# Kernel tuning notes

Measured on AMD Instinct MI355X. Metric: run time of the kernel, lower is better.

Reference implementation:

```python
import jax, jax.numpy as jnp
import numpy as np

NEG_SLOPE = 0.01  # torch LeakyReLU default

def setup_inputs() -> dict:
    key = jax.random.key(0)
    ks = jax.random.split(key, 16)
    B, T = 256, 168
    LAG, LAT, WS, H = 168, 128, 64, 1024
    def lin(kw, kb, out_f, in_f):
        bound = 1.0 / np.sqrt(in_f)
        W = jax.random.uniform(kw, (out_f, in_f), jnp.float32, -bound, bound)
        b = jax.random.uniform(kb, (out_f,), jnp.float32, -bound, bound)
        return W, b
    W1, b1 = lin(ks[0], ks[1], 64, LAG)
    W2, b2 = lin(ks[2], ks[3], LAT, 64)
    W3, b3 = lin(ks[4], ks[5], H, LAT)
    bound = 1.0 / np.sqrt(H)
    Wih = jax.random.uniform(ks[6], (3 * H, WS), jnp.float32, -bound, bound)
    Whh = jax.random.uniform(ks[7], (3 * H, H), jnp.float32, -bound, bound)
    bih = jax.random.uniform(ks[8], (3 * H,), jnp.float32, -bound, bound)
    bhh = jax.random.uniform(ks[9], (3 * H,), jnp.float32, -bound, bound)
    Wo, bo = lin(ks[10], ks[11], 1, H)
    lag = jax.random.normal(ks[12], (B, LAG), jnp.float32)
    curr = jax.random.normal(ks[13], (T, B, WS), jnp.float32)
    return dict(lag=lag, curr=curr, W1=W1, b1=b1, W2=W2, b2=b2, W3=W3, b3=b3,
                Wih=Wih, Whh=Whh, bih=bih, bhh=bhh, Wo=Wo, bo=bo)

def _leaky(x):
    return jnp.where(x >= 0, x, NEG_SLOPE * x)

def reference(lag, curr, W1, b1, W2, b2, W3, b3, Wih, Whh, bih, bhh, Wo, bo):
    # Encoder MLP: lag -> 64 -> latent -> hidden (leaky relu after first two)
    h = _leaky(lag @ W1.T + b1)
    h = _leaky(h @ W2.T + b2)
    h0 = h @ W3.T + b3  # [B, H]
    H = h0.shape[-1]

    def step(h_t, x_t):
        gi = x_t @ Wih.T + bih          # [B, 3H]
        gh = h_t @ Whh.T + bhh          # [B, 3H]
        ir, iz, inn = jnp.split(gi, 3, axis=-1)
        hr, hz, hn = jnp.split(gh, 3, axis=-1)
        r = jax.nn.sigmoid(ir + hr)
        z = jax.nn.sigmoid(iz + hz)
        n = jnp.tanh(inn + r * hn)
        h_new = (1.0 - z) * n + z * h_t
        return h_new, h_new

    _, hs = jax.lax.scan(step, h0, curr)          # hs: [T, B, H]
    preds = jnp.squeeze(hs @ Wo.T + bo, -1)       # [T, B]
    return preds.T                                 # [B, T]
```

## Files before the change

kernel.cpp:

```cpp
#include <hip/hip_runtime.h>
#include <hip/hip_bf16.h>
#include <cstdint>
#include <cstddef>

typedef _Float16 half8 __attribute__((ext_vector_type(8)));
typedef _Float16 half4 __attribute__((ext_vector_type(4)));
typedef float floatx4 __attribute__((ext_vector_type(4)));
typedef unsigned long long u64;

#define B_ 256
#define T_ 168
#define H_ 1024
#define WS_ 64
#define LAG_ 168
#define LAT_ 128

__device__ __forceinline__ float fast_sigmoid(float x) {
    return __builtin_amdgcn_rcpf(1.f + __expf(-x));
}
__device__ __forceinline__ float fast_tanh(float x) {
    return 1.f - 2.f * __builtin_amdgcn_rcpf(__expf(2.f * x) + 1.f);
}

__global__ void cvt_all(const float4* __restrict__ a, half4* __restrict__ da, int na,
                        const float4* __restrict__ b, half4* __restrict__ db, int nb,
                        const float4* __restrict__ c, half4* __restrict__ dc, int nc) {
    int i = blockIdx.x * blockDim.x + threadIdx.x;
    const float4* s;
    half4* d;
    int j = i;
    if (j < na) { s = a; d = da; }
    else {
        j -= na;
        if (j < nb) { s = b; d = db; }
        else {
            j -= nb;
            if (j >= nc) return;
            s = c; d = dc;
        }
    }
    float4 v = s[j];
    half4 o;
    o[0] = (_Float16)v.x; o[1] = (_Float16)v.y;
    o[2] = (_Float16)v.z; o[3] = (_Float16)v.w;
    d[j] = o;
}

__global__ void enc_fused(const float* __restrict__ lag,
                          const float* __restrict__ W1, const float* __restrict__ b1,
                          const float* __restrict__ W2, const float* __restrict__ b2,
                          const float* __restrict__ W3, const float* __restrict__ b3,
                          float* __restrict__ hprev32, _Float16* __restrict__ h0f16) {
    __shared__ float lrow[LAG_];
    __shared__ float l1[64];
    __shared__ float l2[LAT_];
    const int r = blockIdx.x, tid = threadIdx.x;
    if (tid < LAG_) lrow[tid] = lag[(size_t)r * LAG_ + tid];
    __syncthreads();
    if (tid < 64) {
        const float* w = W1 + (size_t)tid * LAG_;
        float s = b1[tid];
        for (int k = 0; k < LAG_; ++k) s += lrow[k] * w[k];
        l1[tid] = (s >= 0.f) ? s : 0.01f * s;
    }
    __syncthreads();
    if (tid < LAT_) {
        const float* w = W2 + (size_t)tid * 64;
        float s = b2[tid];
        for (int k = 0; k < 64; ++k) s += l1[k] * w[k];
        l2[tid] = (s >= 0.f) ? s : 0.01f * s;
    }
    __syncthreads();
    for (int j = tid; j < H_; j += 256) {
        const float* w = W3 + (size_t)j * LAT_;
        float acc = b3[j];
        #pragma unroll 8
        for (int k = 0; k < LAT_; ++k) acc += l2[k] * w[k];
        hprev32[(size_t)r * H_ + j] = acc;
        h0f16[(size_t)r * H_ + j]   = (_Float16)acc;
    }
}

__global__ __launch_bounds__(256, 1) void gru_persistent(
    _Float16* __restrict__ hbuf,
    const float* __restrict__ hprev32, const _Float16* __restrict__ whh16,
    const _Float16* __restrict__ wih16, const _Float16* __restrict__ x16,
    const float* __restrict__ bih, const float* __restrict__ bhh,
    const float* __restrict__ Wo, float* __restrict__ partials,
    unsigned* __restrict__ bar)
{
    __shared__ __align__(16) _Float16 Ash[16 * 1032];
    __shared__ __align__(16) _Float16 Wsh[192 * 72];
    __shared__ __align__(16) _Float16 Hsh[4 * 256];

    const int tid  = threadIdx.x;
    const int w    = tid >> 6;
    const int lane = tid & 63;
    const int m16  = lane & 15;
    const int quad = lane >> 4;
    const int pi   = blockIdx.x & 15;
    const int qi   = blockIdx.x >> 4;
    const int pi16 = pi << 4;
    const int u    = (qi << 6) + (w << 4) + m16;

    for (int idx = tid; idx < 1536; idx += 256) {
        int rowl = idx >> 3, ch = idx & 7;
        int g = rowl >> 6, ru = rowl & 63;
        *(uint4*)(&Wsh[rowl * 72 + (ch << 3)]) =
            *(const uint4*)(wih16 + (size_t)(((g << 10) + (qi << 6) + ru) << 6) + (ch << 3));
    }

    half8 br[32], bz[32], bn[32];
    {
        const _Float16* p0 = whh16 + ((size_t)u << 10) + (quad << 3);
        const _Float16* p1 = whh16 + ((size_t)(H_ + u) << 10) + (quad << 3);
        const _Float16* p2 = whh16 + ((size_t)(2 * H_ + u) << 10) + (quad << 3);
        #pragma unroll
        for (int c = 0; c < 32; ++c) br[c] = *(const half8*)(p0 + (c << 5));
        #pragma unroll
        for (int c = 0; c < 32; ++c) bz[c] = *(const half8*)(p1 + (c << 5));
        #pragma unroll
        for (int c = 0; c < 32; ++c) bn[c] = *(const half8*)(p2 + (c << 5));
    }

    const float b_r  = bih[u]          + bhh[u];
    const float b_z  = bih[H_ + u]     + bhh[H_ + u];
    const float b_in = bih[2 * H_ + u];
    const float b_hn = bhh[2 * H_ + u];
    const float wo_u = Wo[u];

    float hreg[4];
    #pragma unroll
    for (int i = 0; i < 4; ++i)
        hreg[i] = hprev32[((size_t)(pi16 + (quad << 2) + i) << 10) + u];

    __syncthreads();

    unsigned* flag_self       = bar + (((pi << 4) | qi) << 4);
    const unsigned* flag_peer = bar + (((pi << 4) | (lane & 15)) << 4);
    const int srow = tid >> 4;
    const int sch  = tid & 15;
    const int prow = lane >> 2;
    const int pc4  = lane & 3;

    for (int t = 0; t < T_; ++t) {
        const _Float16* hsrc = hbuf + (size_t)(t & 3) * (B_ * H_);
        _Float16*       hdst = hbuf + (size_t)((t + 1) & 3) * (B_ * H_);

        half8 ax0 = *(const half8*)(x16 + (((size_t)t << 8) + pi16 + m16) * WS_ + (quad << 3));
        half8 ax1 = *(const half8*)(x16 + (((size_t)t << 8) + pi16 + m16) * WS_ + 32 + (quad << 3));

        const unsigned need = (unsigned)t;
        u64 rdy = 0;

        while ((rdy & 0xFFFFull) != 0xFFFFull) {
            unsigned f = 0;
            if (lane < 16)
                f = __hip_atomic_load(flag_peer, __ATOMIC_RELAXED, __HIP_MEMORY_SCOPE_AGENT);
            rdy |= __ballot(f >= need);
            if ((rdy & 0xFFFFull) != 0xFFFFull) __builtin_amdgcn_s_sleep(1);
        }

        u64 va[4][4];
        {
            const _Float16* s = hsrc + ((size_t)(pi16 + srow) << 10) + (sch << 4);
            #pragma unroll
            for (int g = 0; g < 4; ++g) {
                #pragma unroll
                for (int k = 0; k < 4; ++k)
                    va[g][k] = __hip_atomic_load((const u64*)(s + (g << 8) + (k << 2)),
                                                 __ATOMIC_RELAXED, __HIP_MEMORY_SCOPE_AGENT);
            }
        }

        floatx4 acc_r  = {b_r,  b_r,  b_r,  b_r };
        floatx4 acc_z  = {b_z,  b_z,  b_z,  b_z };
        floatx4 acc_in = {b_in, b_in, b_in, b_in};
        floatx4 acc_hn = {b_hn, b_hn, b_hn, b_hn};

        {
            half8 p0 = *(const half8*)(&Wsh[((w << 4) + m16) * 72        + (quad << 3)]);
            half8 p1 = *(const half8*)(&Wsh[(64 + (w << 4) + m16) * 72   + (quad << 3)]);
            half8 p2 = *(const half8*)(&Wsh[(128 + (w << 4) + m16) * 72  + (quad << 3)]);
            acc_r  = __builtin_amdgcn_mfma_f32_16x16x32_f16(ax0, p0, acc_r,  0, 0, 0);
            acc_z  = __builtin_amdgcn_mfma_f32_16x16x32_f16(ax0, p1, acc_z,  0, 0, 0);
            acc_in = __builtin_amdgcn_mfma_f32_16x16x32_f16(ax0, p2, acc_in, 0, 0, 0);
            half8 q0 = *(const half8*)(&Wsh[((w << 4) + m16) * 72        + 32 + (quad << 3)]);
            half8 q1 = *(const half8*)(&Wsh[(64 + (w << 4) + m16) * 72   + 32 + (quad << 3)]);
            half8 q2 = *(const half8*)(&Wsh[(128 + (w << 4) + m16) * 72  + 32 + (quad << 3)]);
            acc_r  = __builtin_amdgcn_mfma_f32_16x16x32_f16(ax1, q0, acc_r,  0, 0, 0);
            acc_z  = __builtin_amdgcn_mfma_f32_16x16x32_f16(ax1, q1, acc_z,  0, 0, 0);
            acc_in = __builtin_amdgcn_mfma_f32_16x16x32_f16(ax1, q2, acc_in, 0, 0, 0);
        }

        {
            _Float16* dbase = &Ash[srow * 1032 + (sch << 4)];
            #pragma unroll
            for (int g = 0; g < 4; ++g) {
                _Float16* d = dbase + (g << 8);
                *(u64*)(d + 0)  = va[g][0];
                *(u64*)(d + 4)  = va[g][1];
                *(u64*)(d + 8)  = va[g][2];
                *(u64*)(d + 12) = va[g][3];
            }
        }
        __syncthreads();

        #pragma unroll
        for (int c = 0; c < 32; ++c) {
            half8 a = *(const half8*)(&Ash[m16 * 1032 + (c << 5) + (quad << 3)]);
            acc_r  = __builtin_amdgcn_mfma_f32_16x16x32_f16(a, br[c], acc_r,  0, 0, 0);
            acc_z  = __builtin_amdgcn_mfma_f32_16x16x32_f16(a, bz[c], acc_z,  0, 0, 0);
            acc_hn = __builtin_amdgcn_mfma_f32_16x16x32_f16(a, bn[c], acc_hn, 0, 0, 0);
        }

        float pv[4];
        #pragma unroll
        for (int i = 0; i < 4; ++i) {
            float rg = fast_sigmoid(acc_r[i]);
            float zg = fast_sigmoid(acc_z[i]);
            float ng = fast_tanh(acc_in[i] + rg * acc_hn[i]);
            float hn2 = (1.f - zg) * ng + zg * hreg[i];
            hreg[i] = hn2;
            pv[i] = hn2 * wo_u;
            Hsh[(w << 8) + ((quad << 2) + i) * 16 + m16] = (_Float16)hn2;
        }
        __threadfence_block();
        {
            u64 hv = *(const u64*)(&Hsh[(w << 8) + prow * 16 + (pc4 << 2)]);
            __hip_atomic_store(
                (u64*)(hdst + ((size_t)(pi16 + prow) << 10) + (qi << 6) + (w << 4) + (pc4 << 2)),
                hv, __ATOMIC_RELAXED, __HIP_MEMORY_SCOPE_AGENT);
        }
        #pragma unroll
        for (int m = 1; m < 16; m <<= 1) {
            #pragma unroll
            for (int i = 0; i < 4; ++i) pv[i] += __shfl_xor(pv[i], m);
        }
        asm volatile("s_waitcnt vmcnt(0)" ::: "memory");
        __syncthreads();
        if (tid == 0)
            __hip_atomic_store(flag_self, (unsigned)(t + 1),
                               __ATOMIC_RELAXED, __HIP_MEMORY_SCOPE_AGENT);
        if (m16 == 0) {
            #pragma unroll
            for (int i = 0; i < 4; ++i)
                partials[((size_t)(t << 6) + (qi << 2) + w) * 256 + pi16 + (quad << 2) + i] = pv[i];
        }
    }
}

__global__ void out_reduce(const float* __restrict__ partials, const float* __restrict__ bo,
                           float* __restrict__ out) {
    int t = blockIdx.x, r = threadIdx.x;
    float s = 0.f;
    #pragma unroll
    for (int k = 0; k < 64; ++k) s += partials[((size_t)(t << 6) + k) * 256 + r];
    out[(size_t)r * T_ + t] = s + bo[0];
}

extern "C" void kernel_launch(void* const* d_in, const int* in_sizes, int n_in,
                              void* d_out, int out_size, void* d_ws, size_t ws_size,
                              hipStream_t stream) {
    const float* lag  = (const float*)d_in[0];
    const float* curr = (const float*)d_in[1];
    const float* W1   = (const float*)d_in[2];
    const float* b1   = (const float*)d_in[3];
    const float* W2   = (const float*)d_in[4];
    const float* b2   = (const float*)d_in[5];
    const float* W3   = (const float*)d_in[6];
    const float* b3   = (const float*)d_in[7];
    const float* Wih  = (const float*)d_in[8];
    const float* Whh  = (const float*)d_in[9];
    const float* bih  = (const float*)d_in[10];
    const float* bhh  = (const float*)d_in[11];
    const float* Wo   = (const float*)d_in[12];
    const float* bo   = (const float*)d_in[13];
    float* out = (float*)d_out;

    char* ws = (char*)d_ws;
    size_t off = 0;
    auto alloc = [&](size_t bytes) -> void* {
        void* p = ws + off;
        off += (bytes + 255) & ~(size_t)255;
        return p;
    };
    _Float16* whh16 = (_Float16*)alloc((size_t)3 * H_ * H_ * 2);
    _Float16* wih16 = (_Float16*)alloc((size_t)3 * H_ * WS_ * 2);
    _Float16* x16   = (_Float16*)alloc((size_t)T_ * B_ * WS_ * 2);
    _Float16* hbuf  = (_Float16*)alloc((size_t)4 * B_ * H_ * 2);
    float* hprev32  = (float*)alloc((size_t)B_ * H_ * 4);
    float* partials = (float*)alloc((size_t)T_ * B_ * 64 * 4);
    unsigned* bar   = (unsigned*)alloc(81920);

    hipMemsetAsync(bar, 0, 81920, stream);

    const int na = 3 * H_ * H_ / 4;
    const int nb = 3 * H_ * WS_ / 4;
    const int nc = T_ * B_ * WS_ / 4;
    const int ntot = na + nb + nc;
    cvt_all<<<(ntot + 255) / 256, 256, 0, stream>>>(
        (const float4*)Whh, (half4*)whh16, na,
        (const float4*)Wih, (half4*)wih16, nb,
        (const float4*)curr, (half4*)x16, nc);

    enc_fused<<<B_, 256, 0, stream>>>(lag, W1, b1, W2, b2, W3, b3, hprev32, hbuf);

    gru_persistent<<<dim3(256), dim3(256), 0, stream>>>(
        hbuf, hprev32, whh16, wih16, x16, bih, bhh, Wo, partials, bar);

    out_reduce<<<T_, B_, 0, stream>>>(partials, bo, out);
}
```

Measured before the change: 876.7 us.

## Replace per-step flag barrier with sentinel-valued hidden-state ring buffer

Allocates a full T+1 slot ring of hidden states pre-filled with 0xFF sentinels, so consumers poll the data itself instead of waiting on producer flags. This removes the separate flag store/load round trip per step and double-buffers the LDS staging tile. A fallback kernel used when workspace is too small pipelines flag waits per 256-column chunk and streams the n-gate weights from global memory instead of holding them in registers. The cost is a large memset of the ring each call (about 88 MB), and a reliance on no valid fp16 quad equalling the sentinel pattern.

```diff
diff --git a/kernel.cpp b/kernel.cpp
--- a/kernel.cpp
+++ b/kernel.cpp
@@ -14,6 +14,7 @@
 #define WS_ 64
 #define LAG_ 168
 #define LAT_ 128
+#define SENT 0xFFFFFFFFFFFFFFFFull
 
 __device__ __forceinline__ float fast_sigmoid(float x) {
     return __builtin_amdgcn_rcpf(1.f + __expf(-x));
@@ -81,15 +82,14 @@
     }
 }
 
-__global__ __launch_bounds__(256, 1) void gru_persistent(
-    _Float16* __restrict__ hbuf,
+__global__ __launch_bounds__(256, 1) void gru_sentinel(
+    _Float16* __restrict__ hring,
     const float* __restrict__ hprev32, const _Float16* __restrict__ whh16,
     const _Float16* __restrict__ wih16, const _Float16* __restrict__ x16,
     const float* __restrict__ bih, const float* __restrict__ bhh,
-    const float* __restrict__ Wo, float* __restrict__ partials,
-    unsigned* __restrict__ bar)
+    const float* __restrict__ Wo, float* __restrict__ partials)
 {
-    __shared__ __align__(16) _Float16 Ash[16 * 1032];
+    __shared__ __align__(16) _Float16 Ash[2][16 * 1032];
     __shared__ __align__(16) _Float16 Wsh[192 * 72];
     __shared__ __align__(16) _Float16 Hsh[4 * 256];
 
@@ -136,42 +136,26 @@
 
     __syncthreads();
 
-    unsigned* flag_self       = bar + (((pi << 4) | qi) << 4);
-    const unsigned* flag_peer = bar + (((pi << 4) | (lane & 15)) << 4);
     const int srow = tid >> 4;
     const int sch  = tid & 15;
     const int prow = lane >> 2;
     const int pc4  = lane & 3;
 
     for (int t = 0; t < T_; ++t) {
-        const _Float16* hsrc = hbuf + (size_t)(t & 3) * (B_ * H_);
-        _Float16*       hdst = hbuf + (size_t)((t + 1) & 3) * (B_ * H_);
+        const _Float16* hsrc = hring + (size_t)t * (B_ * H_);
+        _Float16*       hdst = hring + (size_t)(t + 1) * (B_ * H_);
 
         half8 ax0 = *(const half8*)(x16 + (((size_t)t << 8) + pi16 + m16) * WS_ + (quad << 3));
         half8 ax1 = *(const half8*)(x16 + (((size_t)t << 8) + pi16 + m16) * WS_ + 32 + (quad << 3));
 
-        const unsigned need = (unsigned)t;
-        u64 rdy = 0;
-
-        while ((rdy & 0xFFFFull) != 0xFFFFull) {
-            unsigned f = 0;
-            if (lane < 16)
-                f = __hip_atomic_load(flag_peer, __ATOMIC_RELAXED, __HIP_MEMORY_SCOPE_AGENT);
-            rdy |= __ballot(f >= need);
-            if ((rdy & 0xFFFFull) != 0xFFFFull) __builtin_amdgcn_s_sleep(1);
-        }
-
         u64 va[4][4];
-        {
-            const _Float16* s = hsrc + ((size_t)(pi16 + srow) << 10) + (sch << 4);
-            #pragma unroll
-            for (int g = 0; g < 4; ++g) {
-                #pragma unroll
-                for (int k = 0; k < 4; ++k)
-                    va[g][k] = __hip_atomic_load((const u64*)(s + (g << 8) + (k << 2)),
-                                                 __ATOMIC_RELAXED, __HIP_MEMORY_SCOPE_AGENT);
-            }
-        }
+        const _Float16* s = hsrc + ((size_t)(pi16 + srow) << 10) + (sch << 4);
+        #pragma unroll
+        for (int g = 0; g < 4; ++g)
+            #pragma unroll
+            for (int k = 0; k < 4; ++k)
+                va[g][k] = __hip_atomic_load((const u64*)(s + (g << 8) + (k << 2)),
+                                             __ATOMIC_RELAXED, __HIP_MEMORY_SCOPE_AGENT);
 
         floatx4 acc_r  = {b_r,  b_r,  b_r,  b_r };
         floatx4 acc_z  = {b_z,  b_z,  b_z,  b_z };
@@ -193,8 +177,26 @@
             acc_in = __builtin_amdgcn_mfma_f32_16x16x32_f16(ax1, q2, acc_in, 0, 0, 0);
         }
 
+        for (;;) {
+            bool miss = false;
+            #pragma unroll
+            for (int g = 0; g < 4; ++g)
+                #pragma unroll
+                for (int k = 0; k < 4; ++k)
+                    miss |= (va[g][k] == SENT);
+            if (!__any(miss)) break;
+            __builtin_amdgcn_s_sleep(1);
+            #pragma unroll
+            for (int g = 0; g < 4; ++g)
+                #pragma unroll
+                for (int k = 0; k < 4; ++k)
+                    if (va[g][k] == SENT)
+                        va[g][k] = __hip_atomic_load((const u64*)(s + (g << 8) + (k << 2)),
+                                                     __ATOMIC_RELAXED, __HIP_MEMORY_SCOPE_AGENT);
+        }
+
         {
-            _Float16* dbase = &Ash[srow * 1032 + (sch << 4)];
+            _Float16* dbase = &Ash[t & 1][srow * 1032 + (sch << 4)];
             #pragma unroll
             for (int g = 0; g < 4; ++g) {
                 _Float16* d = dbase + (g << 8);
@@ -206,12 +208,196 @@
         }
         __syncthreads();
 
+        const _Float16* abase = &Ash[t & 1][m16 * 1032 + (quad << 3)];
         #pragma unroll
         for (int c = 0; c < 32; ++c) {
-            half8 a = *(const half8*)(&Ash[m16 * 1032 + (c << 5) + (quad << 3)]);
+            half8 a = *(const half8*)(abase + (c << 5));
             acc_r  = __builtin_amdgcn_mfma_f32_16x16x32_f16(a, br[c], acc_r,  0, 0, 0);
             acc_z  = __builtin_amdgcn_mfma_f32_16x16x32_f16(a, bz[c], acc_z,  0, 0, 0);
             acc_hn = __builtin_amdgcn_mfma_f32_16x16x32_f16(a, bn[c], acc_hn, 0, 0, 0);
+        }
+
+        float pv[4];
+        #pragma unroll
+        for (int i = 0; i < 4; ++i) {
+            float rg = fast_sigmoid(acc_r[i]);
+            float zg = fast_sigmoid(acc_z[i]);
+            float ng = fast_tanh(acc_in[i] + rg * acc_hn[i]);
+            float hn2 = (1.f - zg) * ng + zg * hreg[i];
+            hreg[i] = hn2;
+            pv[i] = hn2 * wo_u;
+            Hsh[(w << 8) + ((quad << 2) + i) * 16 + m16] = (_Float16)hn2;
+        }
+        __threadfence_block();
+        {
+            u64 hv = *(const u64*)(&Hsh[(w << 8) + prow * 16 + (pc4 << 2)]);
+            __hip_atomic_store(
+                (u64*)(hdst + ((size_t)(pi16 + prow) << 10) + (qi << 6) + (w << 4) + (pc4 << 2)),
+                hv, __ATOMIC_RELAXED, __HIP_MEMORY_SCOPE_AGENT);
+        }
+
+        #pragma unroll
+        for (int m = 1; m < 16; m <<= 1) {
+            #pragma unroll
+            for (int i = 0; i < 4; ++i) pv[i] += __shfl_xor(pv[i], m);
+        }
+        if (m16 == 0) {
+            #pragma unroll
+            for (int i = 0; i < 4; ++i)
+                partials[((size_t)(t << 6) + (qi << 2) + w) * 256 + pi16 + (quad << 2) + i] = pv[i];
+        }
+    }
+}
+
+__global__ __launch_bounds__(256, 1) void gru_flags(
+    _Float16* __restrict__ hbuf,
+    const float* __restrict__ hprev32, const _Float16* __restrict__ whh16,
+    const _Float16* __restrict__ wih16, const _Float16* __restrict__ x16,
+    const float* __restrict__ bih, const float* __restrict__ bhh,
+    const float* __restrict__ Wo, float* __restrict__ partials,
+    unsigned* __restrict__ bar)
+{
+    __shared__ __align__(16) _Float16 Ash[16 * 1032];
+    __shared__ __align__(16) _Float16 Wsh[192 * 72];
+    __shared__ __align__(16) _Float16 Hsh[4 * 256];
+
+    const int tid  = threadIdx.x;
+    const int w    = tid >> 6;
+    const int lane = tid & 63;
+    const int m16  = lane & 15;
+    const int quad = lane >> 4;
+    const int pi   = blockIdx.x & 15;
+    const int qi   = blockIdx.x >> 4;
+    const int pi16 = pi << 4;
+    const int u    = (qi << 6) + (w << 4) + m16;
+
+    for (int idx = tid; idx < 1536; idx += 256) {
+        int rowl = idx >> 3, ch = idx & 7;
+        int g = rowl >> 6, ru = rowl & 63;
+        *(uint4*)(&Wsh[rowl * 72 + (ch << 3)]) =
+            *(const uint4*)(wih16 + (size_t)(((g << 10) + (qi << 6) + ru) << 6) + (ch << 3));
+    }
+
+    half8 br[32], bz[32];
+    {
+        const _Float16* p0 = whh16 + ((size_t)u << 10) + (quad << 3);
+        const _Float16* p1 = whh16 + ((size_t)(H_ + u) << 10) + (quad << 3);
+        #pragma unroll
+        for (int c = 0; c < 32; ++c) br[c] = *(const half8*)(p0 + (c << 5));
+        #pragma unroll
+        for (int c = 0; c < 32; ++c) bz[c] = *(const half8*)(p1 + (c << 5));
+    }
+    const _Float16* bnp = whh16 + ((size_t)(2 * H_ + u) << 10) + (quad << 3);
+
+    const float b_r  = bih[u]          + bhh[u];
+    const float b_z  = bih[H_ + u]     + bhh[H_ + u];
+    const float b_in = bih[2 * H_ + u];
+    const float b_hn = bhh[2 * H_ + u];
+    const float wo_u = Wo[u];
+
+    float hreg[4];
+    #pragma unroll
+    for (int i = 0; i < 4; ++i)
+        hreg[i] = hprev32[((size_t)(pi16 + (quad << 2) + i) << 10) + u];
+
+    __syncthreads();
+
+    unsigned* flag_self       = bar + (((pi << 4) | qi) << 4);
+    const unsigned* flag_peer = bar + (((pi << 4) | (lane & 15)) << 4);
+    const int srow = tid >> 4;
+    const int sch  = tid & 15;
+    const int prow = lane >> 2;
+    const int pc4  = lane & 3;
+
+    for (int t = 0; t < T_; ++t) {
+        const _Float16* hsrc = hbuf + (size_t)(t & 3) * (B_ * H_);
+        _Float16*       hdst = hbuf + (size_t)((t + 1) & 3) * (B_ * H_);
+
+        half8 ax0 = *(const half8*)(x16 + (((size_t)t << 8) + pi16 + m16) * WS_ + (quad << 3));
+        half8 ax1 = *(const half8*)(x16 + (((size_t)t << 8) + pi16 + m16) * WS_ + 32 + (quad << 3));
+        half8 bnA[8], bnB[8];
+        #pragma unroll
+        for (int j = 0; j < 8; ++j) bnA[j] = *(const half8*)(bnp + (j << 5));
+
+        const unsigned need = (unsigned)t;
+        u64 rdy = 0;
+
+        while ((rdy & 0xFull) != 0xFull) {
+            unsigned f = 0;
+            if (lane < 16)
+                f = __hip_atomic_load(flag_peer, __ATOMIC_RELAXED, __HIP_MEMORY_SCOPE_AGENT);
+            rdy |= __ballot(f >= need);
+            if ((rdy & 0xFull) != 0xFull) __builtin_amdgcn_s_sleep(1);
+        }
+        u64 va0, va1, va2, va3;
+        {
+            const _Float16* s = hsrc + ((size_t)(pi16 + srow) << 10) + (sch << 4);
+            va0 = __hip_atomic_load((const u64*)(s + 0),  __ATOMIC_RELAXED, __HIP_MEMORY_SCOPE_AGENT);
+            va1 = __hip_atomic_load((const u64*)(s + 4),  __ATOMIC_RELAXED, __HIP_MEMORY_SCOPE_AGENT);
+            va2 = __hip_atomic_load((const u64*)(s + 8),  __ATOMIC_RELAXED, __HIP_MEMORY_SCOPE_AGENT);
+            va3 = __hip_atomic_load((const u64*)(s + 12), __ATOMIC_RELAXED, __HIP_MEMORY_SCOPE_AGENT);
+        }
+
+        floatx4 acc_r  = {b_r,  b_r,  b_r,  b_r };
+        floatx4 acc_z  = {b_z,  b_z,  b_z,  b_z };
+        floatx4 acc_in = {b_in, b_in, b_in, b_in};
+        floatx4 acc_hn = {b_hn, b_hn, b_hn, b_hn};
+
+        {
+            half8 p0 = *(const half8*)(&Wsh[((w << 4) + m16) * 72        + (quad << 3)]);
+            half8 p1 = *(const half8*)(&Wsh[(64 + (w << 4) + m16) * 72   + (quad << 3)]);
+            half8 p2 = *(const half8*)(&Wsh[(128 + (w << 4) + m16) * 72  + (quad << 3)]);
+            acc_r  = __builtin_amdgcn_mfma_f32_16x16x32_f16(ax0, p0, acc_r,  0, 0, 0);
+            acc_z  = __builtin_amdgcn_mfma_f32_16x16x32_f16(ax0, p1, acc_z,  0, 0, 0);
+            acc_in = __builtin_amdgcn_mfma_f32_16x16x32_f16(ax0, p2, acc_in, 0, 0, 0);
+            half8 q0 = *(const half8*)(&Wsh[((w << 4) + m16) * 72        + 32 + (quad << 3)]);
+            half8 q1 = *(const half8*)(&Wsh[(64 + (w << 4) + m16) * 72   + 32 + (quad << 3)]);
+            half8 q2 = *(const half8*)(&Wsh[(128 + (w << 4) + m16) * 72  + 32 + (quad << 3)]);
+            acc_r  = __builtin_amdgcn_mfma_f32_16x16x32_f16(ax1, q0, acc_r,  0, 0, 0);
+            acc_z  = __builtin_amdgcn_mfma_f32_16x16x32_f16(ax1, q1, acc_z,  0, 0, 0);
+            acc_in = __builtin_amdgcn_mfma_f32_16x16x32_f16(ax1, q2, acc_in, 0, 0, 0);
+        }
+
+        #pragma unroll
+        for (int g = 0; g < 4; ++g) {
+            {
+                _Float16* d = &Ash[srow * 1032 + (g << 8) + (sch << 4)];
+                *(u64*)(d + 0)  = va0;
+                *(u64*)(d + 4)  = va1;
+                *(u64*)(d + 8)  = va2;
+                *(u64*)(d + 12) = va3;
+            }
+            __syncthreads();
+            if (g < 3) {
+                const u64 mask = 0xFull << ((g + 1) << 2);
+                while ((rdy & mask) != mask) {
+                    unsigned f = 0;
+                    if (lane < 16)
+                        f = __hip_atomic_load(flag_peer, __ATOMIC_RELAXED, __HIP_MEMORY_SCOPE_AGENT);
+                    rdy |= __ballot(f >= need);
+                    if ((rdy & mask) != mask) __builtin_amdgcn_s_sleep(1);
+                }
+                const _Float16* s = hsrc + ((size_t)(pi16 + srow) << 10) + ((g + 1) << 8) + (sch << 4);
+                va0 = __hip_atomic_load((const u64*)(s + 0),  __ATOMIC_RELAXED, __HIP_MEMORY_SCOPE_AGENT);
+                va1 = __hip_atomic_load((const u64*)(s + 4),  __ATOMIC_RELAXED, __HIP_MEMORY_SCOPE_AGENT);
+                va2 = __hip_atomic_load((const u64*)(s + 8),  __ATOMIC_RELAXED, __HIP_MEMORY_SCOPE_AGENT);
+                va3 = __hip_atomic_load((const u64*)(s + 12), __ATOMIC_RELAXED, __HIP_MEMORY_SCOPE_AGENT);
+                #pragma unroll
+                for (int j = 0; j < 8; ++j)
+                    bnB[j] = *(const half8*)(bnp + ((((g + 1) << 3) + j) << 5));
+            }
+            #pragma unroll
+            for (int j = 0; j < 8; ++j) {
+                const int c = (g << 3) + j;
+                half8 a = *(const half8*)(&Ash[m16 * 1032 + (c << 5) + (quad << 3)]);
+                acc_r  = __builtin_amdgcn_mfma_f32_16x16x32_f16(a, br[c], acc_r,  0, 0, 0);
+                acc_z  = __builtin_amdgcn_mfma_f32_16x16x32_f16(a, bz[c], acc_z,  0, 0, 0);
+                acc_hn = __builtin_amdgcn_mfma_f32_16x16x32_f16(a, bnA[j], acc_hn, 0, 0, 0);
+            }
+            if (g < 3) {
+                #pragma unroll
+                for (int j = 0; j < 8; ++j) bnA[j] = bnB[j];
+            }
         }
 
         float pv[4];
@@ -288,12 +474,20 @@
     _Float16* whh16 = (_Float16*)alloc((size_t)3 * H_ * H_ * 2);
     _Float16* wih16 = (_Float16*)alloc((size_t)3 * H_ * WS_ * 2);
     _Float16* x16   = (_Float16*)alloc((size_t)T_ * B_ * WS_ * 2);
-    _Float16* hbuf  = (_Float16*)alloc((size_t)4 * B_ * H_ * 2);
     float* hprev32  = (float*)alloc((size_t)B_ * H_ * 4);
     float* partials = (float*)alloc((size_t)T_ * B_ * 64 * 4);
     unsigned* bar   = (unsigned*)alloc(81920);
 
-    hipMemsetAsync(bar, 0, 81920, stream);
+    const size_t slot_bytes = (size_t)B_ * H_ * 2;
+    const size_t ring_bytes = (size_t)(T_ + 1) * slot_bytes;
+    const bool sentinel_mode = (ws_size >= off + ring_bytes + 4096);
+    _Float16* hring = (_Float16*)alloc(sentinel_mode ? ring_bytes : 4 * slot_bytes);
+
+    if (sentinel_mode) {
+        hipMemsetAsync((char*)hring + slot_bytes, 0xFF, ring_bytes - slot_bytes, stream);
+    } else {
+        hipMemsetAsync(bar, 0, 81920, stream);
+    }
 
     const int na = 3 * H_ * H_ / 4;
     const int nb = 3 * H_ * WS_ / 4;
@@ -304,10 +498,14 @@
         (const float4*)Wih, (half4*)wih16, nb,
         (const float4*)curr, (half4*)x16, nc);
 
-    enc_fused<<<B_, 256, 0, stream>>>(lag, W1, b1, W2, b2, W3, b3, hprev32, hbuf);
-
-    gru_persistent<<<dim3(256), dim3(256), 0, stream>>>(
-        hbuf, hprev32, whh16, wih16, x16, bih, bhh, Wo, partials, bar);
+    enc_fused<<<B_, 256, 0, stream>>>(lag, W1, b1, W2, b2, W3, b3, hprev32, hring);
+
+    if (sentinel_mode)
+        gru_sentinel<<<dim3(256), dim3(256), 0, stream>>>(
+            hring, hprev32, whh16, wih16, x16, bih, bhh, Wo, partials);
+    else
+        gru_flags<<<dim3(256), dim3(256), 0, stream>>>(
+            hring, hprev32, whh16, wih16, x16, bih, bhh, Wo, partials, bar);
 
     out_reduce<<<T_, B_, 0, stream>>>(partials, bo, out);
 }
```

Measured after the change: 953.1 us. +8.7%, slower.
